# Performance work log

Measured on AMD Instinct MI355X. Metric: run time of the kernel, lower is better.

Reference implementation:

```python
import jax, jax.numpy as jnp
import numpy as np

E = 200000   # edges (trade events)
N = 20000    # nodes
H = 128      # hidden_dim / memory_dim / time_dim
EF = 32      # edge_feat_dim
T = 14       # price_seq_dim
P = 4        # num_parties
S = 50       # num_states
LH = 32      # LSTM hidden


def setup_inputs() -> dict:
    key = jax.random.key(0)
    ks = jax.random.split(key, 32)
    rn = lambda k, shape, s=0.02: jax.random.normal(k, shape, dtype=jnp.float32) * s
    return {
        'src': jax.random.randint(ks[0], (E,), 0, N),
        'dst': jax.random.randint(ks[1], (E,), 0, N),
        't': jax.random.uniform(ks[2], (E,), dtype=jnp.float32) * 100.0,
        'msg': jax.random.normal(ks[3], (E, EF), dtype=jnp.float32),
        'price_seq': jax.random.normal(ks[4], (E, T), dtype=jnp.float32),
        'trade_t': jax.random.uniform(ks[5], (E,), dtype=jnp.float32),
        'x_static': jax.random.randint(ks[6], (N, 2), 0, P),
        # TGN memory state
        'memory': rn(ks[7], (N, H), 0.05),
        'last_update': jnp.zeros((N,), jnp.float32),
        # time encoder (cos(w*dt + b)), time_dim = H
        'time_w': rn(ks[8], (H,), 1.0),
        'time_b': rn(ks[9], (H,), 1.0),
        # GRU memory updater: input = [mem_src, mem_dst, raw_msg, t_enc] -> 3H+EF
        'gru_Wih': rn(ks[10], (3 * H, 3 * H + EF)),
        'gru_Whh': rn(ks[11], (3 * H, H)),
        'gru_bih': rn(ks[12], (3 * H,)),
        'gru_bhh': rn(ks[13], (3 * H,)),
        # static features
        'party_emb': rn(ks[14], (P, 16), 0.1),
        'state_emb': rn(ks[15], (S, 16), 0.1),
        'static_W': rn(ks[16], (H, 32)),
        'static_b': rn(ks[17], (H,)),
        # price LSTM (input_size=1, hidden=32); torch gate order i,f,g,o
        'lstm_Wih': rn(ks[18], (4 * LH, 1), 0.1),
        'lstm_Whh': rn(ks[19], (4 * LH, LH), 0.1),
        'lstm_bih': rn(ks[20], (4 * LH,), 0.1),
        'lstm_bhh': rn(ks[21], (4 * LH,), 0.1),
        'price_W': rn(ks[22], (H, LH)),
        'price_b': rn(ks[23], (H,)),
        # predictor MLP (dropout inactive at inference)
        'pred_W1': rn(ks[24], (64, 3 * H)),
        'pred_b1': rn(ks[25], (64,)),
        'pred_W2': rn(ks[26], (1, 64)),
        'pred_b2': rn(ks[27], (1,)),
    }


def reference(src, dst, t, msg, price_seq, trade_t, x_static,
              memory, last_update, time_w, time_b,
              gru_Wih, gru_Whh, gru_bih, gru_bhh,
              party_emb, state_emb, static_W, static_b,
              lstm_Wih, lstm_Whh, lstm_bih, lstm_bhh,
              price_W, price_b, pred_W1, pred_b1, pred_W2, pred_b2):
    n_nodes = memory.shape[0]

    # --- TGN memory update: scatter per-edge messages, GRU update, gather ---
    t_enc = lambda dt: jnp.cos(dt[:, None] * time_w[None, :] + time_b)  # [E,H]
    m_src, m_dst = memory[src], memory[dst]
    msg_to_dst = jnp.concatenate([m_src, m_dst, msg, t_enc(t - last_update[dst])], axis=1)
    msg_to_src = jnp.concatenate([m_dst, m_src, msg, t_enc(t - last_update[src])], axis=1)
    idx = jnp.concatenate([dst, src])                       # [2E]
    all_msgs = jnp.concatenate([msg_to_dst, msg_to_src], 0)  # [2E, 3H+EF]
    summed = jax.ops.segment_sum(all_msgs, idx, num_segments=n_nodes)
    count = jax.ops.segment_sum(jnp.ones((idx.shape[0],), jnp.float32), idx, num_segments=n_nodes)
    agg = summed / jnp.maximum(count, 1.0)[:, None]          # mean-aggregated message per node

    # GRUCell(agg, memory), torch semantics
    gi = agg @ gru_Wih.T + gru_bih
    gh = memory @ gru_Whh.T + gru_bhh
    i_r, i_z, i_n = jnp.split(gi, 3, axis=1)
    h_r, h_z, h_n = jnp.split(gh, 3, axis=1)
    r = jax.nn.sigmoid(i_r + h_r)
    z = jax.nn.sigmoid(i_z + h_z)
    n = jnp.tanh(i_n + r * h_n)
    h_new = (1.0 - z) * n + z * memory
    mem_new = jnp.where((count > 0)[:, None], h_new, memory)

    mem_src = mem_new[src]
    mem_dst = mem_new[dst]

    # --- static branch ---
    static_feat = jnp.concatenate([party_emb[x_static[src, 0]], state_emb[x_static[src, 1]]], axis=1)
    src_static = static_feat @ static_W.T + static_b

    # --- price LSTM branch ---
    e, lh = price_seq.shape[0], lstm_Whh.shape[1]

    def step(carry, x_t):
        h, c = carry
        g = x_t @ lstm_Wih.T + lstm_bih + h @ lstm_Whh.T + lstm_bhh
        gi_, gf_, gg_, go_ = jnp.split(g, 4, axis=1)
        c = jax.nn.sigmoid(gf_) * c + jax.nn.sigmoid(gi_) * jnp.tanh(gg_)
        h = jax.nn.sigmoid(go_) * jnp.tanh(c)
        return (h, c), None

    xs = price_seq.T[:, :, None]  # [T, E, 1]
    z0 = jnp.zeros((e, lh), price_seq.dtype)
    (h_n_last, _), _ = jax.lax.scan(step, (z0, z0), xs)
    price_emb = h_n_last @ price_W.T + price_b

    # --- fusion + predictor ---
    pol_ctx = mem_src + src_static
    comp_ctx = mem_dst + price_emb
    combined = jnp.concatenate([pol_ctx, comp_ctx, price_emb], axis=1)
    hid = jax.nn.relu(combined @ pred_W1.T + pred_b1)
    out = hid @ pred_W2.T + pred_b2
    return out.squeeze(-1)
```

## Files before the change

kernel.cpp:

```cpp
#include <hip/hip_runtime.h>

#define H 128
#define EF 32
#define TT 14
#define LH 32
#define KDIM 416
#define GOUT 512
#define KTOT 544
#define KP 288

typedef __attribute__((ext_vector_type(8))) short bf16x8;
typedef __attribute__((ext_vector_type(4))) float f32x4;

__device__ __forceinline__ float sigmoidf_(float x) {
  float e = __builtin_amdgcn_exp2f(x * -1.442695041f);
  return __builtin_amdgcn_rcpf(1.0f + e);
}
__device__ __forceinline__ float tanhfast_(float x) {
  float e = __builtin_amdgcn_exp2f(x * 2.885390082f);
  return 1.0f - 2.0f * __builtin_amdgcn_rcpf(e + 1.0f);
}
__device__ __forceinline__ ushort f2bf(float x) {
  uint u = __float_as_uint(x);
  u += 0x7fff + ((u >> 16) & 1);
  return (ushort)(u >> 16);
}

__global__ __launch_bounds__(256) void pre_kernel(
    const float* __restrict__ Wih, const float* __restrict__ Whh,
    ushort* __restrict__ WcatT,
    const float* __restrict__ W1, const float* __restrict__ b1,
    const float* __restrict__ static_W, const float* __restrict__ static_b,
    const float* __restrict__ price_W, const float* __restrict__ price_b,
    const float* __restrict__ party_emb, const float* __restrict__ state_emb,
    ushort* __restrict__ Wcombb, float* __restrict__ tab_p, float* __restrict__ tab_s,
    float* __restrict__ bias2,
    const float* __restrict__ mem, ushort* __restrict__ mem_b,
    const int* __restrict__ src, const int* __restrict__ dst, int* cnt,
    int E, int N, int nbC, int nbN, int nbB) {
  __shared__ float G1s[4][32];
  int b = blockIdx.x;
  int tid = threadIdx.x;
  if (b < nbC) {
    int total = N * H;
    for (int i = tid + 256 * b; i < total; i += 256 * nbC) mem_b[i] = f2bf(mem[i]);
  } else if (b < nbC + nbN) {
    int cb = b - nbC;
    for (int e = tid + 256 * cb; e < E; e += 256 * nbN) {
      atomicAdd(&cnt[dst[e]], 1);
      atomicAdd(&cnt[src[e]], 1);
    }
  } else if (b < nbC + nbN + nbB) {
    int i = (b - nbC - nbN) * 256 + tid;
    if (i < GOUT * KTOT) {
      int o = i / KTOT, k = i % KTOT;
      int j = o & 127;
      float v = 0.f;
      if (o < 256) {
        int row = (o < 128) ? j : (128 + j);
        v = (k < KDIM) ? Wih[row * KDIM + k] : Whh[row * H + (k - KDIM)];
      } else if (o < 384) {
        v = (k < KDIM) ? Wih[(256 + j) * KDIM + k] : 0.f;
      } else {
        v = (k < KDIM) ? 0.f : Whh[(256 + j) * H + (k - KDIM)];
      }
      WcatT[i] = f2bf(v);
    }
  } else {
    int ob = (b - nbC - nbN - nbB) * 4;
    if (tid < 128) {
      int ol = tid >> 5, k = tid & 31;
      int o = ob + ol;
      float g = 0.f, m = 0.f;
      for (int j = 0; j < 128; j++) {
        g = fmaf(W1[o * 384 + j], static_W[j * 32 + k], g);
        m = fmaf(W1[o * 384 + 128 + j] + W1[o * 384 + 256 + j], price_W[j * 32 + k], m);
      }
      G1s[ol][k] = g;
      Wcombb[o * KP + 256 + k] = f2bf(m);
    }
    for (int idx = tid; idx < 1024; idx += 256) {
      int ol = idx >> 8, j = idx & 255;
      int o = ob + ol;
      Wcombb[o * KP + j] = f2bf(W1[o * 384 + j]);
    }
    __syncthreads();
    for (int idx = tid; idx < 216; idx += 256) {
      if (idx < 16) {
        int p = idx >> 2, ol = idx & 3;
        float s = 0.f;
        for (int k = 0; k < 16; k++) s = fmaf(G1s[ol][k], party_emb[p * 16 + k], s);
        tab_p[p * 64 + ob + ol] = s;
      } else {
        int i2 = idx - 16;
        int si = i2 >> 2, ol = i2 & 3;
        float s = 0.f;
        for (int k = 0; k < 16; k++) s = fmaf(G1s[ol][16 + k], state_emb[si * 16 + k], s);
        tab_s[si * 64 + ob + ol] = s;
      }
    }
    if (tid < 4) {
      int o = ob + tid;
      float s = b1[o];
      for (int j = 0; j < 128; j++) {
        s = fmaf(W1[o * 384 + j], static_b[j], s);
        s = fmaf(W1[o * 384 + 128 + j] + W1[o * 384 + 256 + j], price_b[j], s);
      }
      bias2[o] = s;
    }
  }
}

__global__ __launch_bounds__(1024) void scan_kernel(const int* __restrict__ cnt,
                                                    int* __restrict__ offs,
                                                    int* __restrict__ cursor, int N) {
  __shared__ int part[1024];
  int tid = threadIdx.x;
  int chunk = (N + 1023) / 1024;
  int beg = tid * chunk;
  int end = min(beg + chunk, N);
  int s = 0;
  for (int i = beg; i < end; i++) s += cnt[i];
  part[tid] = s;
  __syncthreads();
  for (int d = 1; d < 1024; d <<= 1) {
    int v = (tid >= d) ? part[tid - d] : 0;
    __syncthreads();
    part[tid] += v;
    __syncthreads();
  }
  int run = (tid > 0) ? part[tid - 1] : 0;
  for (int i = beg; i < end; i++) {
    offs[i] = run;
    cursor[i] = run;
    run += cnt[i];
  }
  if (tid == 1023) offs[N] = part[1023];
}

__global__ void fill_kernel(const int* __restrict__ src, const int* __restrict__ dst,
                            int* cursor, int* __restrict__ other, int* __restrict__ eid, int E) {
  int e = blockIdx.x * blockDim.x + threadIdx.x;
  if (e >= E) return;
  int s = src[e], d = dst[e];
  int p1 = atomicAdd(&cursor[d], 1);
  other[p1] = s; eid[p1] = e;
  int p2 = atomicAdd(&cursor[s], 1);
  other[p2] = d; eid[p2] = e;
}

__global__ __launch_bounds__(512) void agg_lstm_kernel(
    const int* __restrict__ offs, const int* __restrict__ other, const int* __restrict__ eid,
    const float* __restrict__ mem, const ushort* __restrict__ mem_b,
    const float* __restrict__ msg,
    const float* __restrict__ t, const float* __restrict__ lu,
    const float* __restrict__ tw, const float* __restrict__ tb,
    const int* __restrict__ cnt, ushort* __restrict__ agg_b, int N,
    const float* __restrict__ price_seq,
    const float* __restrict__ lWih, const float* __restrict__ lWhh,
    const float* __restrict__ lbih, const float* __restrict__ lbhh,
    ushort* __restrict__ houtb, int E, int nL) {
  __shared__ union {
    struct { int ld_oth[256]; int ld_eid[256]; float red[16 * 292]; } a;
    float ps[128][15];
  } sm;
  int tid = threadIdx.x;

  if ((int)blockIdx.x < nL) {
    int lane = tid & 63;
    int el = lane & 15;
    int g = lane >> 4;
    int wv = tid >> 6;
    int row0 = blockIdx.x * 128;
    int el_local = wv * 16 + el;
    int e = row0 + el_local;
    bool valid = (e < E);

    for (int idx = tid; idx < 128 * TT; idx += 512) {
      int row = idx / TT, col = idx % TT;
      int ee = min(row0 + row, E - 1);
      sm.ps[row][col] = price_seq[(size_t)ee * TT + col];
    }
    __syncthreads();

    union { uint u[4]; bf16x8 v; } afr[8];
#pragma unroll
    for (int bq = 0; bq < 8; bq++) {
      const float* wr = lWhh + (16 * bq + el) * LH + g * 8;
#pragma unroll
      for (int q = 0; q < 4; q++) {
        float lo = wr[2 * q], hi = wr[2 * q + 1];
        asm("v_cvt_pk_bf16_f32 %0, %1, %2" : "=v"(afr[bq].u[q]) : "v"(lo), "v"(hi));
      }
    }
    uint afr2w[8];
#pragma unroll
    for (int bq = 0; bq < 8; bq++) {
      float wvv = lWih[16 * bq + el];
      float bv = lbih[16 * bq + el] + lbhh[16 * bq + el];
      uint pk;
      asm("v_cvt_pk_bf16_f32 %0, %1, %2" : "=v"(pk) : "v"(wvv), "v"(bv));
      afr2w[bq] = (g == 0) ? pk : 0u;
    }

    int addr_i[4];
#pragma unroll
    for (int i = 0; i < 4; i++) addr_i[i] = (el + 16 * ((g & 1) * 2 + (i >> 1))) << 2;
    bool hi_sel = (g >> 1) != 0;

    float cst[8];
#pragma unroll
    for (int i = 0; i < 8; i++) cst[i] = 0.f;
    uint hpk[4] = {0u, 0u, 0u, 0u};
    const f32x4 zero4 = {0.f, 0.f, 0.f, 0.f};

#pragma unroll 1
    for (int tt = 0; tt < TT; tt++) {
      union { uint u[4]; bf16x8 v; } bfr;
#pragma unroll
      for (int i = 0; i < 4; i++) {
        uint lo = (uint)__builtin_amdgcn_ds_bpermute(addr_i[i], (int)hpk[i & 1]);
        uint hi = (uint)__builtin_amdgcn_ds_bpermute(addr_i[i], (int)hpk[2 + (i & 1)]);
        bfr.u[i] = hi_sel ? hi : lo;
      }
      float x = sm.ps[el_local][tt];
      union { uint u[4]; bf16x8 v; } bfr2;
      uint xp;
      asm("v_cvt_pk_bf16_f32 %0, %1, %2" : "=v"(xp) : "v"(x), "v"(1.0f));
      bfr2.u[0] = (g == 0) ? xp : 0u;
      bfr2.u[1] = 0u; bfr2.u[2] = 0u; bfr2.u[3] = 0u;

      float hval[8];
      f32x4 acc0, acc1, acc2, acc3, acc4, acc5, acc6, acc7;
#define STEPACC(bq, A) \
      { union { uint u[4]; bf16x8 v; } a2; a2.u[0] = afr2w[bq]; a2.u[1] = 0u; a2.u[2] = 0u; a2.u[3] = 0u; \
        A = __builtin_amdgcn_mfma_f32_16x16x32_bf16(a2.v, bfr2.v, zero4, 0, 0, 0); \
        A = __builtin_amdgcn_mfma_f32_16x16x32_bf16(afr[bq].v, bfr.v, A, 0, 0, 0); }
      STEPACC(0, acc0) STEPACC(1, acc1) STEPACC(2, acc2) STEPACC(3, acc3)
      STEPACC(4, acc4) STEPACC(5, acc5) STEPACC(6, acc6) STEPACC(7, acc7)
#undef STEPACC
#define NONLIN(b1, AI, AF, AG, AO) \
      { _Pragma("unroll") for (int r = 0; r < 4; r++) { \
          int mi = 4 * b1 + r; \
          float ig = sigmoidf_(AI[r]); \
          float fg = sigmoidf_(AF[r]); \
          float gg = tanhfast_(AG[r]); \
          float og = sigmoidf_(AO[r]); \
          float cv = fmaf(fg, cst[mi], ig * gg); \
          cst[mi] = cv; \
          hval[mi] = og * tanhfast_(cv); } }
      NONLIN(0, acc0, acc2, acc4, acc6)
      NONLIN(1, acc1, acc3, acc5, acc7)
#undef NONLIN
#pragma unroll
      for (int i = 0; i < 4; i++)
        asm("v_cvt_pk_bf16_f32 %0, %1, %2" : "=v"(hpk[i]) : "v"(hval[2 * i]), "v"(hval[2 * i + 1]));
    }

    if (valid) {
      uint2* rowp = reinterpret_cast<uint2*>(houtb + (size_t)e * LH);
      rowp[g] = make_uint2(hpk[0], hpk[1]);
      rowp[4 + g] = make_uint2(hpk[2], hpk[3]);
    }
  } else {
    int grp = tid >> 5;
    int l = tid & 31;
    int v = blockIdx.x - nL;
    int beg = offs[v], end = offs[v + 1];
    int deg = end - beg;
    int ndeg = min(deg, 256);
    for (int i = tid; i < ndeg; i += 512) {
      sm.a.ld_oth[i] = other[beg + i];
      sm.a.ld_eid[i] = eid[beg + i];
    }
    __syncthreads();

    float lupd = lu[v];
    float4 w4 = *reinterpret_cast<const float4*>(tw + 4 * l);
    float4 b4 = *reinterpret_cast<const float4*>(tb + 4 * l);
    float a0q0 = 0.f, a0q1 = 0.f, a0q2 = 0.f, a0q3 = 0.f;
    float ac0 = 0.f, ac1 = 0.f, ac2 = 0.f, ac3 = 0.f;
    float amsg = 0.f;
    for (int p0 = grp; p0 < deg; p0 += 64) {
      int uu[4], ee[4];
      float mk[4];
#pragma unroll
      for (int i = 0; i < 4; i++) {
        int p = p0 + 16 * i;
        bool val = (p < deg);
        int ps = val ? p : p0;
        int u, e;
        if (ps < 256) { u = sm.a.ld_oth[ps]; e = sm.a.ld_eid[ps]; }
        else { u = other[beg + ps]; e = eid[beg + ps]; }
        uu[i] = u; ee[i] = e; mk[i] = val ? 1.f : 0.f;
      }
      uint2 mr[4];
      float tv[4], mg[4];
#pragma unroll
      for (int i = 0; i < 4; i++) {
        mr[i] = *reinterpret_cast<const uint2*>(mem_b + (size_t)uu[i] * H + 4 * l);
        tv[i] = t[ee[i]];
        mg[i] = msg[ee[i] * EF + l];
      }
#pragma unroll
      for (int i = 0; i < 4; i++) {
        float m = mk[i];
        float x0 = __uint_as_float(mr[i].x << 16);
        float x1 = __uint_as_float(mr[i].x & 0xffff0000u);
        float x2 = __uint_as_float(mr[i].y << 16);
        float x3 = __uint_as_float(mr[i].y & 0xffff0000u);
        a0q0 = fmaf(x0, m, a0q0); a0q1 = fmaf(x1, m, a0q1);
        a0q2 = fmaf(x2, m, a0q2); a0q3 = fmaf(x3, m, a0q3);
        float dt = tv[i] - lupd;
        ac0 = fmaf(__cosf(fmaf(dt, w4.x, b4.x)), m, ac0);
        ac1 = fmaf(__cosf(fmaf(dt, w4.y, b4.y)), m, ac1);
        ac2 = fmaf(__cosf(fmaf(dt, w4.z, b4.z)), m, ac2);
        ac3 = fmaf(__cosf(fmaf(dt, w4.w, b4.w)), m, ac3);
        amsg = fmaf(mg[i], m, amsg);
      }
    }
    float* r = sm.a.red + grp * 292;
    r[4 * l + 0] = a0q0; r[4 * l + 1] = a0q1; r[4 * l + 2] = a0q2; r[4 * l + 3] = a0q3;
    r[128 + 4 * l + 0] = ac0; r[128 + 4 * l + 1] = ac1;
    r[128 + 4 * l + 2] = ac2; r[128 + 4 * l + 3] = ac3;
    r[256 + l] = amsg;
    __syncthreads();

    int cv = cnt[v];
    float inv = 1.f / (float)max(cv, 1);
    ushort* arow = agg_b + (size_t)v * KTOT;
    if (tid < 288) {
      float s = 0.f;
#pragma unroll
      for (int g2 = 0; g2 < 16; g2++) s += sm.a.red[g2 * 292 + tid];
      s *= inv;
      if (tid < 128) arow[tid] = f2bf(s);
      else if (tid < 256) arow[288 + (tid - 128)] = f2bf(s);
      else arow[256 + (tid - 256)] = f2bf(s);
    } else if (tid < 416) {
      int c = tid - 288;
      float mv = mem[(size_t)v * H + c];
      arow[128 + c] = f2bf((cv > 0) ? mv : 0.f);
      arow[416 + c] = f2bf(mv);
    }
  }
}

__global__ __launch_bounds__(256) void gru_gemm_mfma(
    const ushort* __restrict__ aggb, const ushort* __restrict__ WcatT,
    const float* __restrict__ mem, const int* __restrict__ cnt,
    const float* __restrict__ bih, const float* __restrict__ bhh,
    ushort* __restrict__ mem_newb, int N) {
  __shared__ union {
    ushort a[32 * 552];
    float g[4][32][132];
  } sm;
  int tid = threadIdx.x;
  int lane = tid & 63;
  int w = tid >> 6;
  int n0 = blockIdx.x * 32;

#pragma unroll
  for (int i = 0; i < 8; i++) {
    int row = w * 8 + i;
    int gr = min(n0 + row, N - 1);
    const uint4* srcp = reinterpret_cast<const uint4*>(aggb + (size_t)gr * KTOT);
    uint4* dstp = reinterpret_cast<uint4*>(sm.a + row * 552);
    dstp[lane] = srcp[lane];
    if (lane < 4) dstp[64 + lane] = srcp[64 + lane];
  }
  __syncthreads();

  f32x4 acc[2][8] = {};
  int arow_b = (lane & 15);
  int koff = (lane >> 4) * 8;
  for (int ks = 0; ks < 17; ks++) {
    int k = ks * 32 + koff;
    bf16x8 afr0 = *reinterpret_cast<const bf16x8*>(sm.a + (arow_b) * 552 + k);
    bf16x8 afr1 = *reinterpret_cast<const bf16x8*>(sm.a + (16 + arow_b) * 552 + k);
#pragma unroll
    for (int nt = 0; nt < 8; nt++) {
      int o = w * 128 + nt * 16 + (lane & 15);
      bf16x8 bfr = *reinterpret_cast<const bf16x8*>(WcatT + (size_t)o * KTOT + k);
      acc[0][nt] = __builtin_amdgcn_mfma_f32_16x16x32_bf16(afr0, bfr, acc[0][nt], 0, 0, 0);
      acc[1][nt] = __builtin_amdgcn_mfma_f32_16x16x32_bf16(afr1, bfr, acc[1][nt], 0, 0, 0);
    }
  }
  __syncthreads();

#pragma unroll
  for (int mt = 0; mt < 2; mt++)
#pragma unroll
    for (int nt = 0; nt < 8; nt++)
#pragma unroll
      for (int r = 0; r < 4; r++)
        sm.g[w][mt * 16 + (lane >> 4) * 4 + r][nt * 16 + (lane & 15)] = acc[mt][nt][r];
  __syncthreads();

  int row = tid >> 3, j0 = (tid & 7) * 16;
  int n = n0 + row;
  if (n < N) {
    int cv = cnt[n];
#pragma unroll
    for (int jj = 0; jj < 16; jj++) {
      int j = j0 + jj;
      float m = mem[(size_t)n * H + j];
      float o;
      if (cv > 0) {
        float rp = sm.g[0][row][j] + bih[j] + bhh[j];
        float zp = sm.g[1][row][j] + bih[128 + j] + bhh[128 + j];
        float ip = sm.g[2][row][j] + bih[256 + j];
        float hp = sm.g[3][row][j] + bhh[256 + j];
        float r = sigmoidf_(rp), z = sigmoidf_(zp);
        float nn = tanhfast_(ip + r * hp);
        o = (1.f - z) * nn + z * m;
      } else {
        o = m;
      }
      mem_newb[(size_t)n * H + j] = f2bf(o);
    }
  }
}

__global__ __launch_bounds__(512) void pred_mfma(
    const int* __restrict__ src, const int* __restrict__ dst,
    const int* __restrict__ x_static,
    const ushort* __restrict__ mem_newb, const ushort* __restrict__ houtb,
    const ushort* __restrict__ Wcombb, const float* __restrict__ tab_p,
    const float* __restrict__ tab_s, const float* __restrict__ bias2,
    const float* __restrict__ W2, const float* __restrict__ b2,
    float* __restrict__ out, int E) {
  __shared__ ushort Asm[128 * 296];
  __shared__ int pidx[128], stix[128];
  __shared__ int sidx[128], didx[128];
  int tid = threadIdx.x;
  int row0 = blockIdx.x * 128;
  if (tid < 128) {
    int e = min(row0 + tid, E - 1);
    int s = src[e], d = dst[e];
    sidx[tid] = s; didx[tid] = d;
    pidx[tid] = x_static[s * 2]; stix[tid] = x_static[s * 2 + 1];
  }
  __syncthreads();
#pragma unroll
  for (int i = 0; i < 9; i++) {
    int idx = tid + i * 512;
    int row = idx / 36, c = idx % 36;
    int e = min(row0 + row, E - 1);
    uint4 v;
    if (c < 16) v = reinterpret_cast<const uint4*>(mem_newb + (size_t)sidx[row] * H)[c];
    else if (c < 32) v = reinterpret_cast<const uint4*>(mem_newb + (size_t)didx[row] * H)[c - 16];
    else v = reinterpret_cast<const uint4*>(houtb + (size_t)e * LH)[c - 32];
    *reinterpret_cast<uint4*>(Asm + row * 296 + c * 8) = v;
  }
  __syncthreads();

  int lane = tid & 63;
  int w = tid >> 6;
  f32x4 acc[4] = {};
  int arow = w * 16 + (lane & 15);
  int koff = (lane >> 4) * 8;
  for (int ks = 0; ks < 9; ks++) {
    int k = ks * 32 + koff;
    bf16x8 afr = *reinterpret_cast<const bf16x8*>(Asm + arow * 296 + k);
#pragma unroll
    for (int nt = 0; nt < 4; nt++) {
      int o = nt * 16 + (lane & 15);
      bf16x8 bfr = *reinterpret_cast<const bf16x8*>(Wcombb + (size_t)o * KP + k);
      acc[nt] = __builtin_amdgcn_mfma_f32_16x16x32_bf16(afr, bfr, acc[nt], 0, 0, 0);
    }
  }
  int ocol = lane & 15;
  float bb2 = b2[0];
#pragma unroll
  for (int r = 0; r < 4; r++) {
    int rl = w * 16 + (lane >> 4) * 4 + r;
    int p = pidx[rl], st = stix[rl];
    float s = 0.f;
#pragma unroll
    for (int nt = 0; nt < 4; nt++) {
      int o = nt * 16 + ocol;
      float hv = acc[nt][r] + bias2[o] + tab_p[p * 64 + o] + tab_s[st * 64 + o];
      s = fmaf(fmaxf(hv, 0.f), W2[o], s);
    }
#pragma unroll
    for (int d = 1; d < 16; d <<= 1) s += __shfl_xor(s, d);
    int e = row0 + rl;
    if (ocol == 0 && e < E) out[e] = s + bb2;
  }
}

extern "C" void kernel_launch(void* const* d_in, const int* in_sizes, int n_in,
                              void* d_out, int out_size, void* d_ws, size_t ws_size,
                              hipStream_t stream) {
  const int* src = (const int*)d_in[0];
  const int* dst = (const int*)d_in[1];
  const float* t = (const float*)d_in[2];
  const float* msg = (const float*)d_in[3];
  const float* price_seq = (const float*)d_in[4];
  const int* x_static = (const int*)d_in[6];
  const float* memory = (const float*)d_in[7];
  const float* last_update = (const float*)d_in[8];
  const float* time_w = (const float*)d_in[9];
  const float* time_b = (const float*)d_in[10];
  const float* gWih = (const float*)d_in[11];
  const float* gWhh = (const float*)d_in[12];
  const float* gbih = (const float*)d_in[13];
  const float* gbhh = (const float*)d_in[14];
  const float* party_emb = (const float*)d_in[15];
  const float* state_emb = (const float*)d_in[16];
  const float* static_W = (const float*)d_in[17];
  const float* static_b = (const float*)d_in[18];
  const float* lWih = (const float*)d_in[19];
  const float* lWhh = (const float*)d_in[20];
  const float* lbih = (const float*)d_in[21];
  const float* lbhh = (const float*)d_in[22];
  const float* price_W = (const float*)d_in[23];
  const float* price_b = (const float*)d_in[24];
  const float* W1 = (const float*)d_in[25];
  const float* b1 = (const float*)d_in[26];
  const float* W2 = (const float*)d_in[27];
  const float* b2 = (const float*)d_in[28];
  float* out = (float*)d_out;

  const int E = in_sizes[0];
  const int N = in_sizes[8];

  char* ws = (char*)d_ws;
  size_t off = 0;
  auto alloc = [&](size_t bytes) { size_t o = off; off += (bytes + 255) & ~(size_t)255; return o; };
  int* cnt       = (int*)(ws + alloc((size_t)N * 4));
  int* offs      = (int*)(ws + alloc((size_t)(N + 1) * 4));
  int* cursor    = (int*)(ws + alloc((size_t)N * 4));
  int* other     = (int*)(ws + alloc((size_t)2 * E * 4));
  int* eid       = (int*)(ws + alloc((size_t)2 * E * 4));
  ushort* WcatT  = (ushort*)(ws + alloc((size_t)GOUT * KTOT * 2));
  ushort* Wcombb = (ushort*)(ws + alloc((size_t)64 * KP * 2));
  float* tab_p   = (float*)(ws + alloc((size_t)4 * 64 * 4));
  float* tab_s   = (float*)(ws + alloc((size_t)50 * 64 * 4));
  float* bias2   = (float*)(ws + alloc((size_t)64 * 4));
  ushort* agg_b  = (ushort*)(ws + alloc((size_t)N * KTOT * 2));
  ushort* mem_newb = (ushort*)(ws + alloc((size_t)N * H * 2));
  ushort* houtb  = (ushort*)(ws + alloc((size_t)E * LH * 2));
  ushort* mem_b  = (ushort*)(ws + alloc((size_t)N * H * 2));
  (void)ws_size;

  hipMemsetAsync(cnt, 0, (size_t)N * 4, stream);

  int nbC = 128, nbN = 128, nbB = (GOUT * KTOT + 255) / 256, nbP = 16;
  pre_kernel<<<nbC + nbN + nbB + nbP, 256, 0, stream>>>(
      gWih, gWhh, WcatT, W1, b1, static_W, static_b, price_W, price_b,
      party_emb, state_emb, Wcombb, tab_p, tab_s, bias2,
      memory, mem_b, src, dst, cnt, E, N, nbC, nbN, nbB);
  scan_kernel<<<1, 1024, 0, stream>>>(cnt, offs, cursor, N);
  fill_kernel<<<(E + 255) / 256, 256, 0, stream>>>(src, dst, cursor, other, eid, E);
  int nL = (E + 127) / 128;
  agg_lstm_kernel<<<nL + N, 512, 0, stream>>>(offs, other, eid, memory, mem_b, msg, t,
                                              last_update, time_w, time_b, cnt, agg_b, N,
                                              price_seq, lWih, lWhh, lbih, lbhh, houtb, E, nL);
  gru_gemm_mfma<<<(N + 31) / 32, 256, 0, stream>>>(agg_b, WcatT, memory, cnt,
                                                   gbih, gbhh, mem_newb, N);
  pred_mfma<<<(E + 127) / 128, 512, 0, stream>>>(src, dst, x_static, mem_newb, houtb,
      Wcombb, tab_p, tab_s, bias2, W2, b2, out, E);
}
```

Baseline: 419.3 us.

## Move LSTM into preprocessing kernel and keep GRU gate epilogue in registers

The price LSTM blocks move out of the aggregation kernel and into the preprocessing kernel, now launched with 512 threads. The LSTM work then runs alongside the weight/count preprocessing instead of competing with the per-node aggregation blocks. The GRU GEMM output tiles are redistributed so each wave owns matching r/z/n columns across all four gate groups. This lets the gate nonlinearity run straight from accumulator registers and drops the shared-memory staging buffer and two barriers. The cost is more accumulator registers per thread in the GRU kernel and less coalesced epilogue stores.

```diff
diff --git a/kernel.cpp b/kernel.cpp
--- a/kernel.cpp
+++ b/kernel.cpp
@@ -26,8 +26,8 @@
   return (ushort)(u >> 16);
 }
 
-__global__ __launch_bounds__(256) void pre_kernel(
-    const float* __restrict__ Wih, const float* __restrict__ Whh,
+__global__ __launch_bounds__(512) void pre_lstm_kernel(
+    const float* __restrict__ gWih, const float* __restrict__ gWhh,
     ushort* __restrict__ WcatT,
     const float* __restrict__ W1, const float* __restrict__ b1,
     const float* __restrict__ static_W, const float* __restrict__ static_b,
@@ -37,36 +37,45 @@
     float* __restrict__ bias2,
     const float* __restrict__ mem, ushort* __restrict__ mem_b,
     const int* __restrict__ src, const int* __restrict__ dst, int* cnt,
-    int E, int N, int nbC, int nbN, int nbB) {
-  __shared__ float G1s[4][32];
+    const float* __restrict__ price_seq,
+    const float* __restrict__ lWih, const float* __restrict__ lWhh,
+    const float* __restrict__ lbih, const float* __restrict__ lbhh,
+    ushort* __restrict__ houtb,
+    int E, int N, int nbC, int nbN, int nbB, int nbP) {
+  __shared__ union {
+    float ps[128][15];
+    float G1s[4][32];
+  } sm;
   int b = blockIdx.x;
   int tid = threadIdx.x;
+  int nbPre = nbC + nbN + nbB + nbP;
+
   if (b < nbC) {
     int total = N * H;
-    for (int i = tid + 256 * b; i < total; i += 256 * nbC) mem_b[i] = f2bf(mem[i]);
+    for (int i = tid + 512 * b; i < total; i += 512 * nbC) mem_b[i] = f2bf(mem[i]);
   } else if (b < nbC + nbN) {
     int cb = b - nbC;
-    for (int e = tid + 256 * cb; e < E; e += 256 * nbN) {
+    for (int e = tid + 512 * cb; e < E; e += 512 * nbN) {
       atomicAdd(&cnt[dst[e]], 1);
       atomicAdd(&cnt[src[e]], 1);
     }
   } else if (b < nbC + nbN + nbB) {
-    int i = (b - nbC - nbN) * 256 + tid;
+    int i = (b - nbC - nbN) * 512 + tid;
     if (i < GOUT * KTOT) {
       int o = i / KTOT, k = i % KTOT;
       int j = o & 127;
       float v = 0.f;
       if (o < 256) {
         int row = (o < 128) ? j : (128 + j);
-        v = (k < KDIM) ? Wih[row * KDIM + k] : Whh[row * H + (k - KDIM)];
+        v = (k < KDIM) ? gWih[row * KDIM + k] : gWhh[row * H + (k - KDIM)];
       } else if (o < 384) {
-        v = (k < KDIM) ? Wih[(256 + j) * KDIM + k] : 0.f;
+        v = (k < KDIM) ? gWih[(256 + j) * KDIM + k] : 0.f;
       } else {
-        v = (k < KDIM) ? 0.f : Whh[(256 + j) * H + (k - KDIM)];
+        v = (k < KDIM) ? 0.f : gWhh[(256 + j) * H + (k - KDIM)];
       }
       WcatT[i] = f2bf(v);
     }
-  } else {
+  } else if (b < nbPre) {
     int ob = (b - nbC - nbN - nbB) * 4;
     if (tid < 128) {
       int ol = tid >> 5, k = tid & 31;
@@ -76,26 +85,26 @@
         g = fmaf(W1[o * 384 + j], static_W[j * 32 + k], g);
         m = fmaf(W1[o * 384 + 128 + j] + W1[o * 384 + 256 + j], price_W[j * 32 + k], m);
       }
-      G1s[ol][k] = g;
+      sm.G1s[ol][k] = g;
       Wcombb[o * KP + 256 + k] = f2bf(m);
     }
-    for (int idx = tid; idx < 1024; idx += 256) {
+    for (int idx = tid; idx < 1024; idx += 512) {
       int ol = idx >> 8, j = idx & 255;
       int o = ob + ol;
       Wcombb[o * KP + j] = f2bf(W1[o * 384 + j]);
     }
     __syncthreads();
-    for (int idx = tid; idx < 216; idx += 256) {
+    for (int idx = tid; idx < 216; idx += 512) {
       if (idx < 16) {
         int p = idx >> 2, ol = idx & 3;
         float s = 0.f;
-        for (int k = 0; k < 16; k++) s = fmaf(G1s[ol][k], party_emb[p * 16 + k], s);
+        for (int k = 0; k < 16; k++) s = fmaf(sm.G1s[ol][k], party_emb[p * 16 + k], s);
         tab_p[p * 64 + ob + ol] = s;
       } else {
         int i2 = idx - 16;
         int si = i2 >> 2, ol = i2 & 3;
         float s = 0.f;
-        for (int k = 0; k < 16; k++) s = fmaf(G1s[ol][16 + k], state_emb[si * 16 + k], s);
+        for (int k = 0; k < 16; k++) s = fmaf(sm.G1s[ol][16 + k], state_emb[si * 16 + k], s);
         tab_s[si * 64 + ob + ol] = s;
       }
     }
@@ -107,6 +116,103 @@
         s = fmaf(W1[o * 384 + 128 + j] + W1[o * 384 + 256 + j], price_b[j], s);
       }
       bias2[o] = s;
+    }
+  } else {
+    int lb = b - nbPre;
+    int lane = tid & 63;
+    int el = lane & 15;
+    int g = lane >> 4;
+    int wv = tid >> 6;
+    int row0 = lb * 128;
+    int el_local = wv * 16 + el;
+    int e = row0 + el_local;
+    bool valid = (e < E);
+
+    for (int idx = tid; idx < 128 * TT; idx += 512) {
+      int row = idx / TT, col = idx % TT;
+      int ee = min(row0 + row, E - 1);
+      sm.ps[row][col] = price_seq[(size_t)ee * TT + col];
+    }
+    __syncthreads();
+
+    union { uint u[4]; bf16x8 v; } afr[8];
+#pragma unroll
+    for (int bq = 0; bq < 8; bq++) {
+      const float* wr = lWhh + (16 * bq + el) * LH + g * 8;
+#pragma unroll
+      for (int q = 0; q < 4; q++) {
+        float lo = wr[2 * q], hi = wr[2 * q + 1];
+        asm("v_cvt_pk_bf16_f32 %0, %1, %2" : "=v"(afr[bq].u[q]) : "v"(lo), "v"(hi));
+      }
+    }
+    uint afr2w[8];
+#pragma unroll
+    for (int bq = 0; bq < 8; bq++) {
+      float wvv = lWih[16 * bq + el];
+      float bv = lbih[16 * bq + el] + lbhh[16 * bq + el];
+      uint pk;
+      asm("v_cvt_pk_bf16_f32 %0, %1, %2" : "=v"(pk) : "v"(wvv), "v"(bv));
+      afr2w[bq] = (g == 0) ? pk : 0u;
+    }
+
+    int addr_i[4];
+#pragma unroll
+    for (int i = 0; i < 4; i++) addr_i[i] = (el + 16 * ((g & 1) * 2 + (i >> 1))) << 2;
+    bool hi_sel = (g >> 1) != 0;
+
+    float cst[8];
+#pragma unroll
+    for (int i = 0; i < 8; i++) cst[i] = 0.f;
+    uint hpk[4] = {0u, 0u, 0u, 0u};
+    const f32x4 zero4 = {0.f, 0.f, 0.f, 0.f};
+
+#pragma unroll 1
+    for (int tt = 0; tt < TT; tt++) {
+      union { uint u[4]; bf16x8 v; } bfr;
+#pragma unroll
+      for (int i = 0; i < 4; i++) {
+        uint lo = (uint)__builtin_amdgcn_ds_bpermute(addr_i[i], (int)hpk[i & 1]);
+        uint hi = (uint)__builtin_amdgcn_ds_bpermute(addr_i[i], (int)hpk[2 + (i & 1)]);
+        bfr.u[i] = hi_sel ? hi : lo;
+      }
+      float x = sm.ps[el_local][tt];
+      union { uint u[4]; bf16x8 v; } bfr2;
+      uint xp;
+      asm("v_cvt_pk_bf16_f32 %0, %1, %2" : "=v"(xp) : "v"(x), "v"(1.0f));
+      bfr2.u[0] = (g == 0) ? xp : 0u;
+      bfr2.u[1] = 0u; bfr2.u[2] = 0u; bfr2.u[3] = 0u;
+
+      float hval[8];
+      f32x4 acc0, acc1, acc2, acc3, acc4, acc5, acc6, acc7;
+#define STEPACC(bq, A) \
+      { union { uint u[4]; bf16x8 v; } a2; a2.u[0] = afr2w[bq]; a2.u[1] = 0u; a2.u[2] = 0u; a2.u[3] = 0u; \
+        A = __builtin_amdgcn_mfma_f32_16x16x32_bf16(a2.v, bfr2.v, zero4, 0, 0, 0); \
+        A = __builtin_amdgcn_mfma_f32_16x16x32_bf16(afr[bq].v, bfr.v, A, 0, 0, 0); }
+      STEPACC(0, acc0) STEPACC(1, acc1) STEPACC(2, acc2) STEPACC(3, acc3)
+      STEPACC(4, acc4) STEPACC(5, acc5) STEPACC(6, acc6) STEPACC(7, acc7)
+#undef STEPACC
+#define NONLIN(b1q, AI, AF, AG, AO) \
+      { _Pragma("unroll") for (int r = 0; r < 4; r++) { \
+          int mi = 4 * b1q + r; \
+          float ig = sigmoidf_(AI[r]); \
+          float fg = sigmoidf_(AF[r]); \
+          float gg = tanhfast_(AG[r]); \
+          float og = sigmoidf_(AO[r]); \
+          float cv = fmaf(fg, cst[mi], ig * gg); \
+          cst[mi] = cv; \
+          hval[mi] = og * tanhfast_(cv); } }
+      NONLIN(0, acc0, acc2, acc4, acc6)
+      NONLIN(1, acc1, acc3, acc5, acc7)
+#undef NONLIN
+#pragma unroll
+      for (int i = 0; i < 4; i++)
+        asm("v_cvt_pk_bf16_f32 %0, %1, %2" : "=v"(hpk[i]) : "v"(hval[2 * i]), "v"(hval[2 * i + 1]));
+    }
+
+    if (valid) {
+      uint2* rowp = reinterpret_cast<uint2*>(houtb + (size_t)e * LH);
+      rowp[g] = make_uint2(hpk[0], hpk[1]);
+      rowp[4 + g] = make_uint2(hpk[2], hpk[3]);
     }
   }
 }
@@ -149,200 +255,96 @@
   other[p2] = d; eid[p2] = e;
 }
 
-__global__ __launch_bounds__(512) void agg_lstm_kernel(
+__global__ __launch_bounds__(512) void agg_kernel(
     const int* __restrict__ offs, const int* __restrict__ other, const int* __restrict__ eid,
     const float* __restrict__ mem, const ushort* __restrict__ mem_b,
     const float* __restrict__ msg,
     const float* __restrict__ t, const float* __restrict__ lu,
     const float* __restrict__ tw, const float* __restrict__ tb,
-    const int* __restrict__ cnt, ushort* __restrict__ agg_b, int N,
-    const float* __restrict__ price_seq,
-    const float* __restrict__ lWih, const float* __restrict__ lWhh,
-    const float* __restrict__ lbih, const float* __restrict__ lbhh,
-    ushort* __restrict__ houtb, int E, int nL) {
-  __shared__ union {
-    struct { int ld_oth[256]; int ld_eid[256]; float red[16 * 292]; } a;
-    float ps[128][15];
-  } sm;
+    const int* __restrict__ cnt, ushort* __restrict__ agg_b, int N) {
+  __shared__ int ld_oth[256];
+  __shared__ int ld_eid[256];
+  __shared__ float red[16 * 292];
   int tid = threadIdx.x;
-
-  if ((int)blockIdx.x < nL) {
-    int lane = tid & 63;
-    int el = lane & 15;
-    int g = lane >> 4;
-    int wv = tid >> 6;
-    int row0 = blockIdx.x * 128;
-    int el_local = wv * 16 + el;
-    int e = row0 + el_local;
-    bool valid = (e < E);
-
-    for (int idx = tid; idx < 128 * TT; idx += 512) {
-      int row = idx / TT, col = idx % TT;
-      int ee = min(row0 + row, E - 1);
-      sm.ps[row][col] = price_seq[(size_t)ee * TT + col];
-    }
-    __syncthreads();
-
-    union { uint u[4]; bf16x8 v; } afr[8];
-#pragma unroll
-    for (int bq = 0; bq < 8; bq++) {
-      const float* wr = lWhh + (16 * bq + el) * LH + g * 8;
-#pragma unroll
-      for (int q = 0; q < 4; q++) {
-        float lo = wr[2 * q], hi = wr[2 * q + 1];
-        asm("v_cvt_pk_bf16_f32 %0, %1, %2" : "=v"(afr[bq].u[q]) : "v"(lo), "v"(hi));
-      }
-    }
-    uint afr2w[8];
-#pragma unroll
-    for (int bq = 0; bq < 8; bq++) {
-      float wvv = lWih[16 * bq + el];
-      float bv = lbih[16 * bq + el] + lbhh[16 * bq + el];
-      uint pk;
-      asm("v_cvt_pk_bf16_f32 %0, %1, %2" : "=v"(pk) : "v"(wvv), "v"(bv));
-      afr2w[bq] = (g == 0) ? pk : 0u;
-    }
-
-    int addr_i[4];
-#pragma unroll
-    for (int i = 0; i < 4; i++) addr_i[i] = (el + 16 * ((g & 1) * 2 + (i >> 1))) << 2;
-    bool hi_sel = (g >> 1) != 0;
-
-    float cst[8];
-#pragma unroll
-    for (int i = 0; i < 8; i++) cst[i] = 0.f;
-    uint hpk[4] = {0u, 0u, 0u, 0u};
-    const f32x4 zero4 = {0.f, 0.f, 0.f, 0.f};
-
-#pragma unroll 1
-    for (int tt = 0; tt < TT; tt++) {
-      union { uint u[4]; bf16x8 v; } bfr;
-#pragma unroll
-      for (int i = 0; i < 4; i++) {
-        uint lo = (uint)__builtin_amdgcn_ds_bpermute(addr_i[i], (int)hpk[i & 1]);
-        uint hi = (uint)__builtin_amdgcn_ds_bpermute(addr_i[i], (int)hpk[2 + (i & 1)]);
-        bfr.u[i] = hi_sel ? hi : lo;
-      }
-      float x = sm.ps[el_local][tt];
-      union { uint u[4]; bf16x8 v; } bfr2;
-      uint xp;
-      asm("v_cvt_pk_bf16_f32 %0, %1, %2" : "=v"(xp) : "v"(x), "v"(1.0f));
-      bfr2.u[0] = (g == 0) ? xp : 0u;
-      bfr2.u[1] = 0u; bfr2.u[2] = 0u; bfr2.u[3] = 0u;
-
-      float hval[8];
-      f32x4 acc0, acc1, acc2, acc3, acc4, acc5, acc6, acc7;
-#define STEPACC(bq, A) \
-      { union { uint u[4]; bf16x8 v; } a2; a2.u[0] = afr2w[bq]; a2.u[1] = 0u; a2.u[2] = 0u; a2.u[3] = 0u; \
-        A = __builtin_amdgcn_mfma_f32_16x16x32_bf16(a2.v, bfr2.v, zero4, 0, 0, 0); \
-        A = __builtin_amdgcn_mfma_f32_16x16x32_bf16(afr[bq].v, bfr.v, A, 0, 0, 0); }
-      STEPACC(0, acc0) STEPACC(1, acc1) STEPACC(2, acc2) STEPACC(3, acc3)
-      STEPACC(4, acc4) STEPACC(5, acc5) STEPACC(6, acc6) STEPACC(7, acc7)
-#undef STEPACC
-#define NONLIN(b1, AI, AF, AG, AO) \
-      { _Pragma("unroll") for (int r = 0; r < 4; r++) { \
-          int mi = 4 * b1 + r; \
-          float ig = sigmoidf_(AI[r]); \
-          float fg = sigmoidf_(AF[r]); \
-          float gg = tanhfast_(AG[r]); \
-          float og = sigmoidf_(AO[r]); \
-          float cv = fmaf(fg, cst[mi], ig * gg); \
-          cst[mi] = cv; \
-          hval[mi] = og * tanhfast_(cv); } }
-      NONLIN(0, acc0, acc2, acc4, acc6)
-      NONLIN(1, acc1, acc3, acc5, acc7)
-#undef NONLIN
-#pragma unroll
-      for (int i = 0; i < 4; i++)
-        asm("v_cvt_pk_bf16_f32 %0, %1, %2" : "=v"(hpk[i]) : "v"(hval[2 * i]), "v"(hval[2 * i + 1]));
-    }
-
-    if (valid) {
-      uint2* rowp = reinterpret_cast<uint2*>(houtb + (size_t)e * LH);
-      rowp[g] = make_uint2(hpk[0], hpk[1]);
-      rowp[4 + g] = make_uint2(hpk[2], hpk[3]);
-    }
-  } else {
-    int grp = tid >> 5;
-    int l = tid & 31;
-    int v = blockIdx.x - nL;
-    int beg = offs[v], end = offs[v + 1];
-    int deg = end - beg;
-    int ndeg = min(deg, 256);
-    for (int i = tid; i < ndeg; i += 512) {
-      sm.a.ld_oth[i] = other[beg + i];
-      sm.a.ld_eid[i] = eid[beg + i];
-    }
-    __syncthreads();
-
-    float lupd = lu[v];
-    float4 w4 = *reinterpret_cast<const float4*>(tw + 4 * l);
-    float4 b4 = *reinterpret_cast<const float4*>(tb + 4 * l);
-    float a0q0 = 0.f, a0q1 = 0.f, a0q2 = 0.f, a0q3 = 0.f;
-    float ac0 = 0.f, ac1 = 0.f, ac2 = 0.f, ac3 = 0.f;
-    float amsg = 0.f;
-    for (int p0 = grp; p0 < deg; p0 += 64) {
-      int uu[4], ee[4];
-      float mk[4];
-#pragma unroll
-      for (int i = 0; i < 4; i++) {
-        int p = p0 + 16 * i;
-        bool val = (p < deg);
-        int ps = val ? p : p0;
-        int u, e;
-        if (ps < 256) { u = sm.a.ld_oth[ps]; e = sm.a.ld_eid[ps]; }
-        else { u = other[beg + ps]; e = eid[beg + ps]; }
-        uu[i] = u; ee[i] = e; mk[i] = val ? 1.f : 0.f;
-      }
-      uint2 mr[4];
-      float tv[4], mg[4];
-#pragma unroll
-      for (int i = 0; i < 4; i++) {
-        mr[i] = *reinterpret_cast<const uint2*>(mem_b + (size_t)uu[i] * H + 4 * l);
-        tv[i] = t[ee[i]];
-        mg[i] = msg[ee[i] * EF + l];
-      }
-#pragma unroll
-      for (int i = 0; i < 4; i++) {
-        float m = mk[i];
-        float x0 = __uint_as_float(mr[i].x << 16);
-        float x1 = __uint_as_float(mr[i].x & 0xffff0000u);
-        float x2 = __uint_as_float(mr[i].y << 16);
-        float x3 = __uint_as_float(mr[i].y & 0xffff0000u);
-        a0q0 = fmaf(x0, m, a0q0); a0q1 = fmaf(x1, m, a0q1);
-        a0q2 = fmaf(x2, m, a0q2); a0q3 = fmaf(x3, m, a0q3);
-        float dt = tv[i] - lupd;
-        ac0 = fmaf(__cosf(fmaf(dt, w4.x, b4.x)), m, ac0);
-        ac1 = fmaf(__cosf(fmaf(dt, w4.y, b4.y)), m, ac1);
-        ac2 = fmaf(__cosf(fmaf(dt, w4.z, b4.z)), m, ac2);
-        ac3 = fmaf(__cosf(fmaf(dt, w4.w, b4.w)), m, ac3);
-        amsg = fmaf(mg[i], m, amsg);
-      }
-    }
-    float* r = sm.a.red + grp * 292;
-    r[4 * l + 0] = a0q0; r[4 * l + 1] = a0q1; r[4 * l + 2] = a0q2; r[4 * l + 3] = a0q3;
-    r[128 + 4 * l + 0] = ac0; r[128 + 4 * l + 1] = ac1;
-    r[128 + 4 * l + 2] = ac2; r[128 + 4 * l + 3] = ac3;
-    r[256 + l] = amsg;
-    __syncthreads();
-
-    int cv = cnt[v];
-    float inv = 1.f / (float)max(cv, 1);
-    ushort* arow = agg_b + (size_t)v * KTOT;
-    if (tid < 288) {
-      float s = 0.f;
-#pragma unroll
-      for (int g2 = 0; g2 < 16; g2++) s += sm.a.red[g2 * 292 + tid];
-      s *= inv;
-      if (tid < 128) arow[tid] = f2bf(s);
-      else if (tid < 256) arow[288 + (tid - 128)] = f2bf(s);
-      else arow[256 + (tid - 256)] = f2bf(s);
-    } else if (tid < 416) {
-      int c = tid - 288;
-      float mv = mem[(size_t)v * H + c];
-      arow[128 + c] = f2bf((cv > 0) ? mv : 0.f);
-      arow[416 + c] = f2bf(mv);
-    }
+  int grp = tid >> 5;
+  int l = tid & 31;
+  int v = blockIdx.x;
+  int beg = offs[v], end = offs[v + 1];
+  int deg = end - beg;
+  int ndeg = min(deg, 256);
+  for (int i = tid; i < ndeg; i += 512) {
+    ld_oth[i] = other[beg + i];
+    ld_eid[i] = eid[beg + i];
+  }
+  __syncthreads();
+
+  float lupd = lu[v];
+  float4 w4 = *reinterpret_cast<const float4*>(tw + 4 * l);
+  float4 b4 = *reinterpret_cast<const float4*>(tb + 4 * l);
+  float a0q0 = 0.f, a0q1 = 0.f, a0q2 = 0.f, a0q3 = 0.f;
+  float ac0 = 0.f, ac1 = 0.f, ac2 = 0.f, ac3 = 0.f;
+  float amsg = 0.f;
+  for (int p0 = grp; p0 < deg; p0 += 64) {
+    int uu[4], ee[4];
+    float mk[4];
+#pragma unroll
+    for (int i = 0; i < 4; i++) {
+      int p = p0 + 16 * i;
+      bool val = (p < deg);
+      int ps = val ? p : p0;
+      int u, e;
+      if (ps < 256) { u = ld_oth[ps]; e = ld_eid[ps]; }
+      else { u = other[beg + ps]; e = eid[beg + ps]; }
+      uu[i] = u; ee[i] = e; mk[i] = val ? 1.f : 0.f;
+    }
+    uint2 mr[4];
+    float tv[4], mg[4];
+#pragma unroll
+    for (int i = 0; i < 4; i++) {
+      mr[i] = *reinterpret_cast<const uint2*>(mem_b + (size_t)uu[i] * H + 4 * l);
+      tv[i] = t[ee[i]];
+      mg[i] = msg[ee[i] * EF + l];
+    }
+#pragma unroll
+    for (int i = 0; i < 4; i++) {
+      float m = mk[i];
+      float x0 = __uint_as_float(mr[i].x << 16);
+      float x1 = __uint_as_float(mr[i].x & 0xffff0000u);
+      float x2 = __uint_as_float(mr[i].y << 16);
+      float x3 = __uint_as_float(mr[i].y & 0xffff0000u);
+      a0q0 = fmaf(x0, m, a0q0); a0q1 = fmaf(x1, m, a0q1);
+      a0q2 = fmaf(x2, m, a0q2); a0q3 = fmaf(x3, m, a0q3);
+      float dt = tv[i] - lupd;
+      ac0 = fmaf(__cosf(fmaf(dt, w4.x, b4.x)), m, ac0);
+      ac1 = fmaf(__cosf(fmaf(dt, w4.y, b4.y)), m, ac1);
+      ac2 = fmaf(__cosf(fmaf(dt, w4.z, b4.z)), m, ac2);
+      ac3 = fmaf(__cosf(fmaf(dt, w4.w, b4.w)), m, ac3);
+      amsg = fmaf(mg[i], m, amsg);
+    }
+  }
+  float* r = red + grp * 292;
+  r[4 * l + 0] = a0q0; r[4 * l + 1] = a0q1; r[4 * l + 2] = a0q2; r[4 * l + 3] = a0q3;
+  r[128 + 4 * l + 0] = ac0; r[128 + 4 * l + 1] = ac1;
+  r[128 + 4 * l + 2] = ac2; r[128 + 4 * l + 3] = ac3;
+  r[256 + l] = amsg;
+  __syncthreads();
+
+  int cv = cnt[v];
+  float inv = 1.f / (float)max(cv, 1);
+  ushort* arow = agg_b + (size_t)v * KTOT;
+  if (tid < 288) {
+    float s = 0.f;
+#pragma unroll
+    for (int g2 = 0; g2 < 16; g2++) s += red[g2 * 292 + tid];
+    s *= inv;
+    if (tid < 128) arow[tid] = f2bf(s);
+    else if (tid < 256) arow[288 + (tid - 128)] = f2bf(s);
+    else arow[256 + (tid - 256)] = f2bf(s);
+  } else if (tid < 416) {
+    int c = tid - 288;
+    float mv = mem[(size_t)v * H + c];
+    arow[128 + c] = f2bf((cv > 0) ? mv : 0.f);
+    arow[416 + c] = f2bf(mv);
   }
 }
 
@@ -351,10 +353,7 @@
     const float* __restrict__ mem, const int* __restrict__ cnt,
     const float* __restrict__ bih, const float* __restrict__ bhh,
     ushort* __restrict__ mem_newb, int N) {
-  __shared__ union {
-    ushort a[32 * 552];
-    float g[4][32][132];
-  } sm;
+  __shared__ ushort As[32 * 552];
   int tid = threadIdx.x;
   int lane = tid & 63;
   int w = tid >> 6;
@@ -365,61 +364,56 @@
     int row = w * 8 + i;
     int gr = min(n0 + row, N - 1);
     const uint4* srcp = reinterpret_cast<const uint4*>(aggb + (size_t)gr * KTOT);
-    uint4* dstp = reinterpret_cast<uint4*>(sm.a + row * 552);
+    uint4* dstp = reinterpret_cast<uint4*>(As + row * 552);
     dstp[lane] = srcp[lane];
     if (lane < 4) dstp[64 + lane] = srcp[64 + lane];
   }
   __syncthreads();
 
-  f32x4 acc[2][8] = {};
+  f32x4 acc[2][4][2] = {};
   int arow_b = (lane & 15);
   int koff = (lane >> 4) * 8;
   for (int ks = 0; ks < 17; ks++) {
     int k = ks * 32 + koff;
-    bf16x8 afr0 = *reinterpret_cast<const bf16x8*>(sm.a + (arow_b) * 552 + k);
-    bf16x8 afr1 = *reinterpret_cast<const bf16x8*>(sm.a + (16 + arow_b) * 552 + k);
-#pragma unroll
-    for (int nt = 0; nt < 8; nt++) {
-      int o = w * 128 + nt * 16 + (lane & 15);
-      bf16x8 bfr = *reinterpret_cast<const bf16x8*>(WcatT + (size_t)o * KTOT + k);
-      acc[0][nt] = __builtin_amdgcn_mfma_f32_16x16x32_bf16(afr0, bfr, acc[0][nt], 0, 0, 0);
-      acc[1][nt] = __builtin_amdgcn_mfma_f32_16x16x32_bf16(afr1, bfr, acc[1][nt], 0, 0, 0);
-    }
-  }
-  __syncthreads();
+    bf16x8 afr0 = *reinterpret_cast<const bf16x8*>(As + (arow_b) * 552 + k);
+    bf16x8 afr1 = *reinterpret_cast<const bf16x8*>(As + (16 + arow_b) * 552 + k);
+#pragma unroll
+    for (int g = 0; g < 4; g++)
+#pragma unroll
+      for (int nt = 0; nt < 2; nt++) {
+        int o = g * 128 + w * 32 + nt * 16 + (lane & 15);
+        bf16x8 bfr = *reinterpret_cast<const bf16x8*>(WcatT + (size_t)o * KTOT + k);
+        acc[0][g][nt] = __builtin_amdgcn_mfma_f32_16x16x32_bf16(afr0, bfr, acc[0][g][nt], 0, 0, 0);
+        acc[1][g][nt] = __builtin_amdgcn_mfma_f32_16x16x32_bf16(afr1, bfr, acc[1][g][nt], 0, 0, 0);
+      }
+  }
 
 #pragma unroll
   for (int mt = 0; mt < 2; mt++)
 #pragma unroll
-    for (int nt = 0; nt < 8; nt++)
-#pragma unroll
-      for (int r = 0; r < 4; r++)
-        sm.g[w][mt * 16 + (lane >> 4) * 4 + r][nt * 16 + (lane & 15)] = acc[mt][nt][r];
-  __syncthreads();
-
-  int row = tid >> 3, j0 = (tid & 7) * 16;
-  int n = n0 + row;
-  if (n < N) {
-    int cv = cnt[n];
-#pragma unroll
-    for (int jj = 0; jj < 16; jj++) {
-      int j = j0 + jj;
-      float m = mem[(size_t)n * H + j];
-      float o;
-      if (cv > 0) {
-        float rp = sm.g[0][row][j] + bih[j] + bhh[j];
-        float zp = sm.g[1][row][j] + bih[128 + j] + bhh[128 + j];
-        float ip = sm.g[2][row][j] + bih[256 + j];
-        float hp = sm.g[3][row][j] + bhh[256 + j];
-        float r = sigmoidf_(rp), z = sigmoidf_(zp);
-        float nn = tanhfast_(ip + r * hp);
-        o = (1.f - z) * nn + z * m;
-      } else {
-        o = m;
-      }
-      mem_newb[(size_t)n * H + j] = f2bf(o);
-    }
-  }
+    for (int r = 0; r < 4; r++) {
+      int n = n0 + mt * 16 + (lane >> 4) * 4 + r;
+      if (n >= N) continue;
+      int cv = cnt[n];
+#pragma unroll
+      for (int nt = 0; nt < 2; nt++) {
+        int j = w * 32 + nt * 16 + (lane & 15);
+        float m = mem[(size_t)n * H + j];
+        float o;
+        if (cv > 0) {
+          float rp = acc[mt][0][nt][r] + bih[j] + bhh[j];
+          float zp = acc[mt][1][nt][r] + bih[128 + j] + bhh[128 + j];
+          float ip = acc[mt][2][nt][r] + bih[256 + j];
+          float hp = acc[mt][3][nt][r] + bhh[256 + j];
+          float rr = sigmoidf_(rp), z = sigmoidf_(zp);
+          float nn = tanhfast_(ip + rr * hp);
+          o = (1.f - z) * nn + z * m;
+        } else {
+          o = m;
+        }
+        mem_newb[(size_t)n * H + j] = f2bf(o);
+      }
+    }
 }
 
 __global__ __launch_bounds__(512) void pred_mfma(
@@ -547,17 +541,19 @@
 
   hipMemsetAsync(cnt, 0, (size_t)N * 4, stream);
 
-  int nbC = 128, nbN = 128, nbB = (GOUT * KTOT + 255) / 256, nbP = 16;
-  pre_kernel<<<nbC + nbN + nbB + nbP, 256, 0, stream>>>(
+  int nbC = 128, nbN = 128, nbB = (GOUT * KTOT + 511) / 512, nbP = 16;
+  int nL = (E + 127) / 128;
+  int nbPre = nbC + nbN + nbB + nbP;
+  pre_lstm_kernel<<<nbPre + nL, 512, 0, stream>>>(
       gWih, gWhh, WcatT, W1, b1, static_W, static_b, price_W, price_b,
       party_emb, state_emb, Wcombb, tab_p, tab_s, bias2,
-      memory, mem_b, src, dst, cnt, E, N, nbC, nbN, nbB);
+      memory, mem_b, src, dst, cnt,
+      price_seq, lWih, lWhh, lbih, lbhh, houtb,
+      E, N, nbC, nbN, nbB, nbP);
   scan_kernel<<<1, 1024, 0, stream>>>(cnt, offs, cursor, N);
   fill_kernel<<<(E + 255) / 256, 256, 0, stream>>>(src, dst, cursor, other, eid, E);
-  int nL = (E + 127) / 128;
-  agg_lstm_kernel<<<nL + N, 512, 0, stream>>>(offs, other, eid, memory, mem_b, msg, t,
-                                              last_update, time_w, time_b, cnt, agg_b, N,
-                                              price_seq, lWih, lWhh, lbih, lbhh, houtb, E, nL);
+  agg_kernel<<<N, 512, 0, stream>>>(offs, other, eid, memory, mem_b, msg, t,
+                                    last_update, time_w, time_b, cnt, agg_b, N);
   gru_gemm_mfma<<<(N + 31) / 32, 256, 0, stream>>>(agg_b, WcatT, memory, cnt,
                                                    gbih, gbhh, mem_newb, N);
   pred_mfma<<<(E + 127) / 128, 512, 0, stream>>>(src, dst, x_static, mem_newb, houtb,
```

Measured after the change: 367.6 us (median of 3 runs). 1.14x faster.
